# Optimization experiments

Hardware: AMD Instinct MI355X
Metric: run time of the kernel (lower is better)

## Reference

```python
import jax, jax.numpy as jnp
import numpy as np

E = 256   # embed_dim
L = 64    # num_landmarks
C = 256   # in_channels
N_ITER = 6


def iterative_inv(K):
    # Newton-Schulz pseudo-inverse on small [*, L, L] matrices (faithful to torch code)
    I = jnp.eye(K.shape[-1], dtype=K.dtype)
    KA = jnp.abs(K)
    V0 = KA.sum(axis=-2, keepdims=True).max(axis=-1, keepdims=True)  # [*,1,1]
    VI = KA.sum(axis=-1, keepdims=True).max(axis=-2, keepdims=True)  # [*,1,1]
    V = jnp.swapaxes(K, -1, -2) / (V0 * VI)
    for _ in range(N_ITER):
        KV = K @ V
        V = 0.25 * V @ (13.0 * I - KV @ (15.0 * I - KV @ (7.0 * I - KV)))
    return V


def setup_inputs() -> dict:
    key = jax.random.key(0)
    k0, k1, k2 = jax.random.split(key, 3)
    x = jax.random.normal(k0, (8, C, 64, 64), dtype=jnp.float32)
    # Conv2d 1x1 weights stored as [out, in]
    w_qkv = jax.random.normal(k1, (3 * E, C), dtype=jnp.float32) * 0.02
    b_qkv = jnp.zeros((3 * E,), dtype=jnp.float32)
    w_out = jax.random.normal(k2, (C, E), dtype=jnp.float32) * 0.02
    b_out = jnp.zeros((C,), dtype=jnp.float32)
    return {"x": x, "w_qkv": w_qkv, "b_qkv": b_qkv, "w_out": w_out, "b_out": b_out}


def reference(x, w_qkv, b_qkv, w_out, b_out):
    N, Cin, H, W = x.shape
    HW = H * W
    # 1x1 conv: [N, 3E, H, W]
    y = jnp.einsum('nchw,ec->nehw', x, w_qkv) + b_qkv[None, :, None, None]
    # faithful raw reshape (mixes channel/spatial like the torch code)
    qkv = y.reshape(N, HW, 3 * E)
    q, k, v = jnp.split(qkv, 3, axis=-1)                     # each [N, HW, E]
    scale = HW ** 0.5
    q_land = q.reshape(N, L, HW // L, E).mean(axis=-2) / scale  # [N, L, E]
    k_land = k.reshape(N, L, HW // L, E).mean(axis=-2) / scale  # [N, L, E]
    # three softmaxes, all over dim=-2 as in the original
    k1 = jax.nn.softmax(jnp.einsum('nie,nje->nij', q, k_land), axis=-2)       # [N, HW, L]
    k2 = jax.nn.softmax(jnp.einsum('nie,nje->nij', q_land, k_land), axis=-2)  # [N, L, L]
    k3 = jax.nn.softmax(jnp.einsum('nie,nje->nij', q_land, k), axis=-2)       # [N, L, HW]
    k2_inv = iterative_inv(k2)
    out = k1 @ (k2_inv @ (k3 @ v)) + v                        # [N, HW, E]
    out = out.reshape(N, E, H, W)                             # faithful raw reshape
    return jnp.einsum('nehw,ce->nchw', out, w_out) + b_out[None, :, None, None]
```

## Files before the change

### kernel.cpp

```cpp
#include <hip/hip_runtime.h>
#include <hip/hip_bf16.h>

typedef unsigned short u16;
typedef __attribute__((ext_vector_type(4))) float f32x4;
typedef __attribute__((ext_vector_type(8))) short short8;

#define NB   8
#define CIN  256
#define EDIM 256
#define M3   768
#define HWN  4096
#define LND  64
#define NS2  72

__device__ __forceinline__ float bf2f(u16 u){ return __uint_as_float(((unsigned)u)<<16); }
__device__ __forceinline__ u16 f2bf(float f){ __hip_bfloat16 h = __float2bfloat16(f); return *reinterpret_cast<u16*>(&h); }
__device__ __forceinline__ void bf2x2(unsigned u, float &lo, float &hi){
  lo = __uint_as_float(u<<16);
  hi = __uint_as_float(u & 0xffff0000u);
}

typedef __attribute__((address_space(1))) unsigned as1_uint;
typedef __attribute__((address_space(3))) unsigned as3_uint;
__device__ __forceinline__ void gl16(const void* g, void* l){
  __builtin_amdgcn_global_load_lds((const as1_uint*)g, (as3_uint*)l, 16, 0, 0);
}

__global__ __launch_bounds__(256) void k_prep(const float* __restrict__ x, u16* __restrict__ Xt,
                                              const float* __restrict__ wq, const float* __restrict__ wo,
                                              u16* __restrict__ Wqb, u16* __restrict__ Wob){
  const int bi = blockIdx.x;
  const int tid = threadIdx.x;
  if(bi >= 2048){
    int ti = (bi-2048)*256 + tid;
    const float* src; u16* dst;
    if(ti < 1536){ src = wq + (size_t)ti*128;        dst = Wqb + (size_t)ti*128; }
    else         { src = wo + (size_t)(ti-1536)*128; dst = Wob + (size_t)(ti-1536)*128; }
    #pragma unroll
    for(int t=0;t<128;t+=8){
      float4 v0 = *(const float4*)(src+t);
      float4 v1 = *(const float4*)(src+t+4);
      ushort4 o0, o1;
      o0.x=f2bf(v0.x); o0.y=f2bf(v0.y); o0.z=f2bf(v0.z); o0.w=f2bf(v0.w);
      o1.x=f2bf(v1.x); o1.y=f2bf(v1.y); o1.z=f2bf(v1.z); o1.w=f2bf(v1.w);
      *(ushort4*)(dst+t)   = o0;
      *(ushort4*)(dst+t+4) = o1;
    }
    return;
  }
  __shared__ float Ts[64*65];
  const int n = bi>>8, rem = bi&255, ct = rem>>6, pt = rem&63;
  const int c0 = ct*64, p0 = pt*64;
  {
    int cc = tid>>2, pj = (tid&3)*16;
    const float* xp = x + (size_t)n*CIN*HWN + (size_t)(c0+cc)*HWN + p0 + pj;
    #pragma unroll
    for(int j=0;j<16;j++) Ts[cc*65 + pj + j] = xp[j];
  }
  __syncthreads();
  {
    int pp = tid>>2, ej = (tid&3)*16;
    u16* op = Xt + ((size_t)n*HWN + p0 + pp)*CIN + c0 + ej;
    ushort4 o[4];
    #pragma unroll
    for(int j=0;j<16;j++) ((u16*)o)[j] = f2bf(Ts[(ej+j)*65 + pp]);
    *(ushort4*)(op+0)  = o[0];
    *(ushort4*)(op+4)  = o[1];
    *(ushort4*)(op+8)  = o[2];
    *(ushort4*)(op+12) = o[3];
  }
}

__global__ __launch_bounds__(256) void k_qkv(const u16* __restrict__ Wb, const u16* __restrict__ Xt,
                                             const float* __restrict__ bias, u16* __restrict__ Y){
  __shared__ __align__(16) u16 As[128*64];
  __shared__ __align__(16) u16 Bs[128*64];
  const int bi = blockIdx.x;
  const int n = bi&7, rem = bi>>3;
  const int ch0 = (rem%6)*128, p0 = (rem/6)*128;
  const int tid = threadIdx.x, lane = tid&63;
  const int c = tid&15, qq = (tid>>4)&3, w4 = tid>>6;
  const int wr0 = (w4&1)*64, wc0 = (w4>>1)*64;
  const u16* xb = Xt + ((size_t)n*HWN + p0)*CIN;
  const u16* wb = Wb + (size_t)ch0*CIN;
  f32x4 acc[4][4];
  #pragma unroll
  for(int mt=0;mt<4;mt++)
    #pragma unroll
    for(int nt=0;nt<4;nt++){ acc[mt][nt][0]=0.f; acc[mt][nt][1]=0.f; acc[mt][nt][2]=0.f; acc[mt][nt][3]=0.f; }
  const int srow  = w4*8 + (lane>>3);
  const int dslot = lane&7;
  const int sgo   = (dslot ^ (lane>>3))*8;
  const int rdswz = (c&7);
  for(int ph=0; ph<4; ph++){
    #pragma unroll
    for(int j=0;j<4;j++){
      int r = j*32 + srow;
      gl16(wb + (size_t)r*CIN + ph*64 + sgo, &As[r*64 + dslot*8]);
    }
    #pragma unroll
    for(int j=0;j<4;j++){
      int r = j*32 + srow;
      gl16(xb + (size_t)r*CIN + ph*64 + sgo, &Bs[r*64 + dslot*8]);
    }
    __syncthreads();
    #pragma unroll
    for(int kt=0;kt<2;kt++){
      short8 af[4], bff[4];
      const int rslot = ((kt*4+qq)^rdswz)*8;
      #pragma unroll
      for(int mt=0;mt<4;mt++) af[mt]  = *(const short8*)&As[(wr0+mt*16+c)*64 + rslot];
      #pragma unroll
      for(int nt=0;nt<4;nt++) bff[nt] = *(const short8*)&Bs[(wc0+nt*16+c)*64 + rslot];
      #pragma unroll
      for(int mt=0;mt<4;mt++)
        #pragma unroll
        for(int nt=0;nt<4;nt++)
          acc[mt][nt] = __builtin_amdgcn_mfma_f32_16x16x32_bf16(af[mt], bff[nt], acc[mt][nt], 0, 0, 0);
    }
    __syncthreads();
  }
  u16* Yb = Y + (size_t)n*M3*HWN;
  #pragma unroll
  for(int mt=0;mt<4;mt++){
    int chb = ch0 + wr0 + mt*16 + 4*qq;
    float b0 = bias[chb], b1 = bias[chb+1], b2 = bias[chb+2], b3 = bias[chb+3];
    #pragma unroll
    for(int nt=0;nt<4;nt++){
      int p = p0 + wc0 + nt*16 + c;
      u16* yp = Yb + (size_t)chb*HWN + p;
      yp[0]             = f2bf(acc[mt][nt][0]+b0);
      yp[HWN]           = f2bf(acc[mt][nt][1]+b1);
      yp[2*(size_t)HWN] = f2bf(acc[mt][nt][2]+b2);
      yp[3*(size_t)HWN] = f2bf(acc[mt][nt][3]+b3);
    }
  }
}

__global__ void k_land(const u16* __restrict__ Y, float* __restrict__ qland, float* __restrict__ kland){
  const int l = blockIdx.x, n = blockIdx.y, e = threadIdx.x;
  const u16* base = Y + (size_t)n*M3*HWN;
  float qs=0.f, ks=0.f;
  #pragma unroll 8
  for(int m=0;m<64;m++){
    size_t off = (size_t)(l*64+m)*M3;
    qs += bf2f(base[off+e]);
    ks += bf2f(base[off+256+e]);
  }
  qland[((size_t)n*LND+l)*EDIM+e] = qs*(1.f/4096.f);
  kland[((size_t)n*LND+l)*EDIM+e] = ks*(1.f/4096.f);
}

__device__ __forceinline__ void ns_mm2(const u16* L, int sL, const u16* Rt, int sR,
                                       int wv, int q, int c, f32x4 r4[4]){
  short8 a0 = *(const short8*)(L + (size_t)(16*wv + c)*sL + 8*q);
  short8 a1 = *(const short8*)(L + (size_t)(16*wv + c)*sL + 32 + 8*q);
  #pragma unroll
  for(int tc=0;tc<4;tc++){
    f32x4 acc = {0.f,0.f,0.f,0.f};
    short8 b0 = *(const short8*)(Rt + (size_t)(16*tc + c)*sR + 8*q);
    short8 b1 = *(const short8*)(Rt + (size_t)(16*tc + c)*sR + 32 + 8*q);
    acc = __builtin_amdgcn_mfma_f32_16x16x32_bf16(a0, b0, acc, 0, 0, 0);
    acc = __builtin_amdgcn_mfma_f32_16x16x32_bf16(a1, b1, acc, 0, 0, 0);
    r4[tc] = acc;
  }
}

#define TTS 64
__device__ void ns_body(int n, char* smem, const float* __restrict__ qland,
                        const float* __restrict__ kland, float* __restrict__ KinvT){
  u16* Kb  = (u16*)(smem + 0);
  u16* Vb  = (u16*)(smem + 9216);
  u16* Vt  = (u16*)(smem + 18432);
  u16* KVb = (u16*)(smem + 27648);
  u16* KVt = (u16*)(smem + 36864);
  u16* Tt  = (u16*)(smem + 46080);
  float* sS   = (float*)(smem + 27648);
  float* sred = (float*)(smem + 44544);
  const int tid = threadIdx.x;
  const int wv = tid>>6, q = (tid>>4)&3, c = tid&15;
  const float* qb = qland + (size_t)n*LND*EDIM;
  const float* kb = kland + (size_t)n*LND*EDIM;
  f32x4 acc[4];
  #pragma unroll
  for(int t=0;t<4;t++){ acc[t][0]=0.f; acc[t][1]=0.f; acc[t][2]=0.f; acc[t][3]=0.f; }
  for(int e0=0;e0<EDIM;e0+=64){
    __syncthreads();
    {
      int row = tid>>2, c0 = (tid&3)*16;
      const float* qp = qb + (size_t)row*EDIM + e0 + c0;
      const float* kp = kb + (size_t)row*EDIM + e0 + c0;
      u16* qd = &KVb[row*NS2 + c0];
      u16* kd = &KVt[row*NS2 + c0];
      #pragma unroll
      for(int j=0;j<16;j+=4){
        float4 qv = *(const float4*)(qp+j);
        float4 kv = *(const float4*)(kp+j);
        ushort4 qo, ko;
        qo.x=f2bf(qv.x); qo.y=f2bf(qv.y); qo.z=f2bf(qv.z); qo.w=f2bf(qv.w);
        ko.x=f2bf(kv.x); ko.y=f2bf(kv.y); ko.z=f2bf(kv.z); ko.w=f2bf(kv.w);
        *(ushort4*)(qd+j) = qo;
        *(ushort4*)(kd+j) = ko;
      }
    }
    __syncthreads();
    {
      short8 a0 = *(const short8*)&KVb[(16*wv+c)*NS2 + 8*q];
      short8 a1 = *(const short8*)&KVb[(16*wv+c)*NS2 + 32 + 8*q];
      #pragma unroll
      for(int tc=0;tc<4;tc++){
        short8 b0 = *(const short8*)&KVt[(16*tc+c)*NS2 + 8*q];
        short8 b1 = *(const short8*)&KVt[(16*tc+c)*NS2 + 32 + 8*q];
        acc[tc] = __builtin_amdgcn_mfma_f32_16x16x32_bf16(a0, b0, acc[tc], 0, 0, 0);
        acc[tc] = __builtin_amdgcn_mfma_f32_16x16x32_bf16(a1, b1, acc[tc], 0, 0, 0);
      }
    }
  }
  __syncthreads();
  #pragma unroll
  for(int tc=0;tc<4;tc++){
    int col = 16*tc + c, row0 = 16*wv + 4*q;
    sS[(row0+0)*66+col] = acc[tc][0];
    sS[(row0+1)*66+col] = acc[tc][1];
    sS[(row0+2)*66+col] = acc[tc][2];
    sS[(row0+3)*66+col] = acc[tc][3];
  }
  __syncthreads();
  if(tid < 64){
    int j = tid;
    float m = -1e30f;
    for(int i=0;i<64;i++) m = fmaxf(m, sS[i*66+j]);
    float ssum = 0.f;
    for(int i=0;i<64;i++) ssum += __expf(sS[i*66+j]-m);
    float inv = 1.f/ssum, cs = 0.f;
    for(int i=0;i<64;i++){
      float kv = __expf(sS[i*66+j]-m)*inv;
      cs += fabsf(kv);
      Kb[i*NS2+j] = f2bf(kv);
    }
    sred[j] = cs;
  }
  __syncthreads();
  if(tid < 64){
    int i = tid; float rs = 0.f;
    for(int j=0;j<64;j++) rs += fabsf(bf2f(Kb[i*NS2+j]));
    sred[64+i] = rs;
  }
  __syncthreads();
  if(tid == 0){
    float v0=-1e30f, vi=-1e30f;
    for(int t=0;t<64;t++){ v0 = fmaxf(v0, sred[t]); vi = fmaxf(vi, sred[64+t]); }
    sred[128] = 1.f/(v0*vi);
  }
  __syncthreads();
  {
    float sc = sred[128];
    int i = tid>>2, j16 = (tid&3)*16;
    #pragma unroll
    for(int jj=0;jj<16;jj++){
      int j = j16+jj;
      u16 bvv = f2bf(bf2f(Kb[j*NS2+i])*sc);
      Vb[i*NS2+j] = bvv;
      Vt[j*NS2+i] = bvv;
    }
  }
  __syncthreads();
  f32x4 r4[4];
  for(int it=0; it<6; it++){
    ns_mm2(Kb, NS2, Vt, NS2, wv, q, c, r4);
    #pragma unroll
    for(int tc=0;tc<4;tc++){
      int col = 16*tc + c, row0 = 16*wv + 4*q;
      ushort4 pk;
      pk.x = f2bf(r4[tc][0]); pk.y = f2bf(r4[tc][1]); pk.z = f2bf(r4[tc][2]); pk.w = f2bf(r4[tc][3]);
      KVb[(row0+0)*NS2+col] = pk.x; KVb[(row0+1)*NS2+col] = pk.y;
      KVb[(row0+2)*NS2+col] = pk.z; KVb[(row0+3)*NS2+col] = pk.w;
      *(ushort4*)&KVt[(size_t)col*NS2 + row0] = pk;
    }
    __syncthreads();
    ns_mm2(KVb, NS2, KVt, NS2, wv, q, c, r4);
    #pragma unroll
    for(int tc=0;tc<4;tc++){
      int col = 16*tc+c, row0 = 16*wv+4*q;
      ushort4 pk;
      #pragma unroll
      for(int r=0;r<4;r++){
        float kvv = bf2f(KVb[(row0+r)*NS2+col]);
        ((u16*)&pk)[r] = f2bf(7.f*kvv - r4[tc][r]);
      }
      *(ushort4*)&Tt[(size_t)col*TTS + row0] = pk;
    }
    __syncthreads();
    ns_mm2(KVb, NS2, Tt, TTS, wv, q, c, r4);
    __syncthreads();
    #pragma unroll
    for(int tc=0;tc<4;tc++){
      int col = 16*tc+c, row0 = 16*wv+4*q;
      ushort4 pk;
      #pragma unroll
      for(int r=0;r<4;r++){
        float kvv = bf2f(KVb[(row0+r)*NS2+col]);
        ((u16*)&pk)[r] = f2bf(15.f*kvv - r4[tc][r]);
      }
      *(ushort4*)&Tt[(size_t)col*TTS + row0] = pk;
    }
    __syncthreads();
    ns_mm2(Vb, NS2, Tt, TTS, wv, q, c, r4);
    __syncthreads();
    #pragma unroll
    for(int tc=0;tc<4;tc++){
      int col = 16*tc+c, row0 = 16*wv+4*q;
      float nv[4]; ushort4 pk;
      #pragma unroll
      for(int r=0;r<4;r++){
        float vv = bf2f(Vb[(row0+r)*NS2+col]);
        nv[r] = 0.25f*(13.f*vv - r4[tc][r]);
        u16 bb = f2bf(nv[r]);
        Vb[(row0+r)*NS2+col] = bb;
        ((u16*)&pk)[r] = bb;
      }
      *(ushort4*)&Vt[(size_t)col*NS2 + row0] = pk;
      if(it==5){
        *(float4*)&KinvT[(size_t)n*4096 + (size_t)col*64 + row0] = make_float4(nv[0],nv[1],nv[2],nv[3]);
      }
    }
    __syncthreads();
  }
}

#define LGS 264
__global__ __launch_bounds__(256) void k_landgemm(const u16* __restrict__ Y, const float* __restrict__ qland,
                                                  const float* __restrict__ kland, float* __restrict__ Z1,
                                                  float* __restrict__ Z3){
  __shared__ __align__(16) u16 As[64*LGS];
  __shared__ __align__(16) u16 BsU[2*64*64];
  const int z = blockIdx.y;
  const int n = z>>1, which = z&1;
  const int b0 = blockIdx.x*64;
  const float* land = (which ? qland : kland) + (size_t)n*LND*EDIM;
  const int boff = which ? 256 : 0;
  float* out = (which ? Z3 : Z1) + (size_t)n*LND*HWN;
  const u16* Yb = Y + (size_t)n*M3*HWN + boff;
  const int tid = threadIdx.x, lane = tid&63;
  const int c = tid&15, qq = (tid>>4)&3, wv = tid>>6;
  {
    int r = tid>>2, c0 = (tid&3)*64;
    const float* lp = land + (size_t)r*EDIM + c0;
    u16* dp = &As[r*LGS + c0];
    #pragma unroll
    for(int j=0;j<64;j+=4){
      float4 v = *(const float4*)(lp+j);
      ushort4 o; o.x=f2bf(v.x); o.y=f2bf(v.y); o.z=f2bf(v.z); o.w=f2bf(v.w);
      *(ushort4*)(dp+j) = o;
    }
  }
  const int srow  = wv*8 + (lane>>3);
  const int dslot = lane&7;
  const int sgo   = (dslot ^ (lane>>3))*8;
  const int rdswz = (c&7);
  f32x4 acc[4];
  #pragma unroll
  for(int nt=0;nt<4;nt++){ acc[nt][0]=0.f; acc[nt][1]=0.f; acc[nt][2]=0.f; acc[nt][3]=0.f; }
  #pragma unroll
  for(int j=0;j<2;j++){
    int r = j*32 + srow;
    gl16(Yb + (size_t)(b0+r)*M3 + sgo, BsU + r*64 + dslot*8);
  }
  __syncthreads();
  for(int ph=0; ph<4; ph++){
    const int cur = ph&1;
    if(ph<3){
      #pragma unroll
      for(int j=0;j<2;j++){
        int r = j*32 + srow;
        gl16(Yb + (size_t)(b0+r)*M3 + (ph+1)*64 + sgo, BsU + (cur^1)*4096 + r*64 + dslot*8);
      }
    }
    #pragma unroll
    for(int kt=0;kt<2;kt++){
      short8 af = *(const short8*)&As[(16*wv + c)*LGS + ph*64 + kt*32 + qq*8];
      const int rslot = ((kt*4+qq)^rdswz)*8;
      #pragma unroll
      for(int nt=0;nt<4;nt++){
        short8 bff = *(const short8*)&BsU[cur*4096 + (nt*16+c)*64 + rslot];
        acc[nt] = __builtin_amdgcn_mfma_f32_16x16x32_bf16(af, bff, acc[nt], 0, 0, 0);
      }
    }
    __syncthreads();
  }
  const int m0 = 16*wv + 4*qq;
  #pragma unroll
  for(int nt=0;nt<4;nt++){
    int col = b0 + nt*16 + c;
    out[(size_t)(m0+0)*HWN + col] = acc[nt][0];
    out[(size_t)(m0+1)*HWN + col] = acc[nt][1];
    out[(size_t)(m0+2)*HWN + col] = acc[nt][2];
    out[(size_t)(m0+3)*HWN + col] = acc[nt][3];
  }
}

__device__ void soft1_body(int b, char* smem, float* __restrict__ Z1){
  const int n = b>>6, j = b&63, tid = threadIdx.x;
  float* redm = (float*)smem;
  float* reds = redm + 4;
  float* base = Z1 + ((size_t)n*LND + j)*HWN;
  float v[16];
  float m = -1e30f;
  #pragma unroll
  for(int r=0;r<16;r++){ v[r] = base[r*256 + tid]; m = fmaxf(m, v[r]); }
  #pragma unroll
  for(int o=32;o;o>>=1) m = fmaxf(m, __shfl_xor(m, o));
  const int wid = tid>>6;
  if((tid&63)==0) redm[wid] = m;
  __syncthreads();
  m = fmaxf(fmaxf(redm[0],redm[1]), fmaxf(redm[2],redm[3]));
  float s = 0.f;
  #pragma unroll
  for(int r=0;r<16;r++){ v[r] = __expf(v[r]-m); s += v[r]; }
  #pragma unroll
  for(int o=32;o;o>>=1) s += __shfl_xor(s, o);
  if((tid&63)==0) reds[wid] = s;
  __syncthreads();
  s = reds[0]+reds[1]+reds[2]+reds[3];
  float inv = 1.f/s;
  #pragma unroll
  for(int r=0;r<16;r++) base[r*256 + tid] = v[r]*inv;
}

__global__ __launch_bounds__(256) void k_pv(const float* __restrict__ Z3, const u16* __restrict__ Y,
                                            float* __restrict__ part, float* __restrict__ Z1,
                                            const float* __restrict__ qland, const float* __restrict__ kland,
                                            float* __restrict__ KinvT){
  __shared__ __align__(16) char smem[54272];
  const int bi = blockIdx.x;
  if(bi < 8){ ns_body(bi, smem, qland, kland, KinvT); return; }
  if(bi >= 520){ soft1_body(bi-520, smem, Z1); return; }
  float* Sf   = (float*)smem;
  float* sinv = (float*)(smem + 33792);
  u16*   Asb  = (u16*)(smem + 34304);
  u16*   Vt   = (u16*)smem;
  const int idx = bi - 8;
  const int kc = idx&31, n = (idx>>5)&7, eh = idx>>8;
  const int jb = kc*128, eb = eh*128;
  const int tid = threadIdx.x, lane = tid&63;
  const int c = tid&15, qq = (tid>>4)&3, wv = tid>>6;
  const u16* Yb = Y + (size_t)n*M3*HWN;
  const float* z3b = Z3 + (size_t)n*LND*HWN;
  {
    int ibase = (tid>>5)*8, j4 = (tid&31)*4;
    #pragma unroll
    for(int r=0;r<8;r++){
      int i = ibase + r;
      *(float4*)&Sf[i*132 + j4] = *(const float4*)&z3b[(size_t)i*HWN + jb + j4];
    }
  }
  __syncthreads();
  if(tid < 128){
    int j = tid;
    float m = -1e30f;
    for(int i=0;i<64;i++) m = fmaxf(m, Sf[i*132 + j]);
    float s = 0.f;
    for(int i=0;i<64;i++){ float e = __expf(Sf[i*132 + j] - m); Sf[i*132 + j] = e; s += e; }
    sinv[j] = 1.f/s;
  }
  __syncthreads();
  {
    int i = tid>>2, j0q = (tid&3)*32;
    const int iswz = (i&7);
    #pragma unroll
    for(int t=0;t<32;t+=4){
      int jg = j0q + t;
      int phb = jg>>6, jl = jg&63;
      ushort4 o;
      o.x = f2bf(Sf[i*132 + jg+0]*sinv[jg+0]);
      o.y = f2bf(Sf[i*132 + jg+1]*sinv[jg+1]);
      o.z = f2bf(Sf[i*132 + jg+2]*sinv[jg+2]);
      o.w = f2bf(Sf[i*132 + jg+3]*sinv[jg+3]);
      *(ushort4*)&Asb[phb*4096 + i*64 + ((jl>>3)^iswz)*8 + (jl&7)] = o;
    }
  }
  __syncthreads();
  const int rdswz = (c&7);
  f32x4 acc[4][2];
  #pragma unroll
  for(int mt=0;mt<4;mt++)
    #pragma unroll
    for(int nt=0;nt<2;nt++){ acc[mt][nt][0]=0.f; acc[mt][nt][1]=0.f; acc[mt][nt][2]=0.f; acc[mt][nt][3]=0.f; }
  for(int ph=0; ph<2; ph++){
    #pragma unroll
    for(int rep=0; rep<4; rep++){
      int jl = (tid>>4) + 16*rep;
      int ec = (tid&15)*8;
      uint4 U = *(const uint4*)&Yb[(size_t)(jb+ph*64+jl)*M3 + 512 + eb + ec];
      const u16* uv = (const u16*)&U;
      #pragma unroll
      for(int k=0;k<8;k++){
        int e = ec+k;
        int slot = ((jl>>3) ^ (e&7) ^ ((e>>3)&7)) & 7;
        Vt[e*64 + slot*8 + (jl&7)] = uv[k];
      }
    }
    __syncthreads();
    #pragma unroll
    for(int kt=0;kt<2;kt++){
      const int rslotA = ((kt*4+qq)^rdswz)*8;
      short8 af[4];
      #pragma unroll
      for(int mt=0;mt<4;mt++) af[mt] = *(const short8*)&Asb[ph*4096 + (mt*16+c)*64 + rslotA];
      #pragma unroll
      for(int nt=0;nt<2;nt++){
        int e = wv*32 + nt*16 + c;
        int slotB = ((kt*4+qq) ^ (e&7) ^ ((e>>3)&7)) & 7;
        short8 bf_ = *(const short8*)&Vt[e*64 + slotB*8];
        #pragma unroll
        for(int mt=0;mt<4;mt++)
          acc[mt][nt] = __builtin_amdgcn_mfma_f32_16x16x32_bf16(af[mt], bf_, acc[mt][nt], 0, 0, 0);
      }
    }
    __syncthreads();
  }
  float* pb = part + ((size_t)n*32 + kc)*LND*EDIM + eb;
  #pragma unroll
  for(int mt=0;mt<4;mt++){
    int row0 = mt*16 + 4*qq;
    #pragma unroll
    for(int nt=0;nt<2;nt++){
      int e = wv*32 + nt*16 + c;
      pb[(size_t)(row0+0)*EDIM + e] = acc[mt][nt][0];
      pb[(size_t)(row0+1)*EDIM + e] = acc[mt][nt][1];
      pb[(size_t)(row0+2)*EDIM + e] = acc[mt][nt][2];
      pb[(size_t)(row0+3)*EDIM + e] = acc[mt][nt][3];
    }
  }
}

__global__ __launch_bounds__(256) void k_c2(const float* __restrict__ KinvT, const float* __restrict__ part,
                                            u16* __restrict__ C2T){
  const int eb = blockIdx.x*64, n = blockIdx.y, tid = threadIdx.x;
  __shared__ float KT[64][68];
  __shared__ float Bs2[64][68];
  __shared__ u16 Ct[64*72];
  {
    int l = tid>>2, o16 = (tid&3)*16;
    const float* kp = KinvT + (size_t)n*4096 + l*64 + o16;
    #pragma unroll
    for(int t=0;t<16;t+=4) *(float4*)&KT[l][o16+t] = *(const float4*)(kp+t);
    const float* pp = part + (size_t)n*32*16384 + (size_t)l*256 + eb + o16;
    float4 s0 = {0,0,0,0}, s1 = {0,0,0,0}, s2 = {0,0,0,0}, s3 = {0,0,0,0};
    for(int kc=0;kc<32;kc++){
      const float* b = pp + (size_t)kc*16384;
      float4 v0 = *(const float4*)(b);
      float4 v1 = *(const float4*)(b+4);
      float4 v2 = *(const float4*)(b+8);
      float4 v3 = *(const float4*)(b+12);
      s0.x+=v0.x; s0.y+=v0.y; s0.z+=v0.z; s0.w+=v0.w;
      s1.x+=v1.x; s1.y+=v1.y; s1.z+=v1.z; s1.w+=v1.w;
      s2.x+=v2.x; s2.y+=v2.y; s2.z+=v2.z; s2.w+=v2.w;
      s3.x+=v3.x; s3.y+=v3.y; s3.z+=v3.z; s3.w+=v3.w;
    }
    *(float4*)&Bs2[l][o16+0]  = s0;
    *(float4*)&Bs2[l][o16+4]  = s1;
    *(float4*)&Bs2[l][o16+8]  = s2;
    *(float4*)&Bs2[l][o16+12] = s3;
  }
  __syncthreads();
  const int j0 = (tid>>4)*4, u0 = (tid&15)*4;
  float acc[4][4] = {};
  #pragma unroll 8
  for(int l=0;l<64;l++){
    f32x4 a = *(f32x4*)&KT[l][j0];
    f32x4 b = *(f32x4*)&Bs2[l][u0];
    #pragma unroll
    for(int s=0;s<4;s++)
      #pragma unroll
      for(int u=0;u<4;u++) acc[s][u] += a[s]*b[u];
  }
  #pragma unroll
  for(int s=0;s<4;s++)
    #pragma unroll
    for(int u=0;u<4;u++)
      Ct[(u0+u)*72 + j0+s] = f2bf(acc[s][u]);
  __syncthreads();
  {
    int e = tid>>2, j16 = (tid&3)*16;
    u16* op = C2T + ((size_t)n*256 + eb + e)*64 + j16;
    #pragma unroll
    for(int t=0;t<16;t+=4)
      *(ushort4*)(op+t) = *(const ushort4*)&Ct[e*72 + j16 + t];
  }
}

__global__ __launch_bounds__(256) void k_out(const float* __restrict__ Z1, const u16* __restrict__ C2T,
                                             const u16* __restrict__ Y, u16* __restrict__ OM){
  __shared__ __align__(16) u16 Cs[256*64];
  __shared__ __align__(16) u16 Zt[64*72];
  const int ib = blockIdx.x*64, n = blockIdx.y;
  const int tid = threadIdx.x, lane = tid&63;
  const int c = tid&15, qq = (tid>>4)&3, wv = tid>>6;
  const int srow  = wv*8 + (lane>>3);
  const int dslot = lane&7;
  const int sgo   = (dslot ^ (lane>>3))*8;
  const int rdswz = (c&7);
  const u16* cb = C2T + (size_t)n*256*64;
  #pragma unroll
  for(int j=0;j<8;j++){
    int r = j*32 + srow;
    gl16(cb + (size_t)r*64 + sgo, &Cs[r*64 + dslot*8]);
  }
  {
    int j = tid>>2, i16 = (tid&3)*16;
    const float* zp = Z1 + ((size_t)n*LND + j)*HWN + ib + i16;
    #pragma unroll
    for(int t=0;t<16;t+=4){
      float4 v = *(const float4*)(zp+t);
      Zt[(i16+t+0)*72 + j] = f2bf(v.x);
      Zt[(i16+t+1)*72 + j] = f2bf(v.y);
      Zt[(i16+t+2)*72 + j] = f2bf(v.z);
      Zt[(i16+t+3)*72 + j] = f2bf(v.w);
    }
  }
  __syncthreads();
  f32x4 acc[4][4];
  #pragma unroll
  for(int mt=0;mt<4;mt++)
    #pragma unroll
    for(int nt=0;nt<4;nt++){ acc[mt][nt][0]=0.f; acc[mt][nt][1]=0.f; acc[mt][nt][2]=0.f; acc[mt][nt][3]=0.f; }
  #pragma unroll
  for(int kt=0;kt<2;kt++){
    const int rslot = ((kt*4+qq)^rdswz)*8;
    short8 af[4], bf_[4];
    #pragma unroll
    for(int mt=0;mt<4;mt++) af[mt] = *(const short8*)&Cs[(wv*64+mt*16+c)*64 + rslot];
    #pragma unroll
    for(int nt=0;nt<4;nt++) bf_[nt] = *(const short8*)&Zt[(nt*16+c)*72 + kt*32 + qq*8];
    #pragma unroll
    for(int mt=0;mt<4;mt++)
      #pragma unroll
      for(int nt=0;nt<4;nt++)
        acc[mt][nt] = __builtin_amdgcn_mfma_f32_16x16x32_bf16(af[mt], bf_[nt], acc[mt][nt], 0, 0, 0);
  }
  const u16* Yb = Y + (size_t)n*M3*HWN;
  u16* ob = OM + (size_t)n*HWN*EDIM;
  #pragma unroll
  for(int mt=0;mt<4;mt++){
    int e = wv*64 + mt*16 + 4*qq;
    #pragma unroll
    for(int nt=0;nt<4;nt++){
      int i = ib + nt*16 + c;
      ushort4 V4 = *(const ushort4*)(Yb + (size_t)i*M3 + 512 + e);
      ushort4 o;
      o.x = f2bf(acc[mt][nt][0] + bf2f(V4.x));
      o.y = f2bf(acc[mt][nt][1] + bf2f(V4.y));
      o.z = f2bf(acc[mt][nt][2] + bf2f(V4.z));
      o.w = f2bf(acc[mt][nt][3] + bf2f(V4.w));
      *(ushort4*)(ob + (size_t)i*EDIM + e) = o;
    }
  }
}

__global__ __launch_bounds__(256) void k_proj(const u16* __restrict__ Wb, const u16* __restrict__ OM,
                                              const float* __restrict__ bias, float* __restrict__ out){
  __shared__ __align__(16) u16 As[128*64];
  __shared__ __align__(16) u16 Bt[128*64];
  const int bi = blockIdx.x;
  const int n = bi&7, rem = bi>>3;
  const int ch0 = (rem&1)*128, p0 = (rem>>1)*128;
  const int tid = threadIdx.x, lane = tid&63;
  const int c = tid&15, qq = (tid>>4)&3, w4 = tid>>6;
  const int wr0 = (w4&1)*64, wc0 = (w4>>1)*64;
  const u16* omb = OM + (size_t)n*HWN*EDIM;
  const u16* wb = Wb + (size_t)ch0*EDIM;
  f32x4 acc[4][4];
  #pragma unroll
  for(int mt=0;mt<4;mt++)
    #pragma unroll
    for(int nt=0;nt<4;nt++){ acc[mt][nt][0]=0.f; acc[mt][nt][1]=0.f; acc[mt][nt][2]=0.f; acc[mt][nt][3]=0.f; }
  const int srow  = w4*8 + (lane>>3);
  const int dslot = lane&7;
  const int sgo   = (dslot ^ (lane>>3))*8;
  const int rdswz = (c&7);
  for(int ph=0; ph<4; ph++){
    #pragma unroll
    for(int j=0;j<4;j++){
      int r = j*32 + srow;
      gl16(wb + (size_t)r*EDIM + ph*64 + sgo, &As[r*64 + dslot*8]);
    }
    #pragma unroll
    for(int rep=0; rep<4; rep++){
      int ee = (tid>>4) + 16*rep;
      int pc = (tid&15)*8;
      uint4 U = *(const uint4*)&omb[(size_t)(ph*64+ee)*HWN + p0 + pc];
      const u16* uv = (const u16*)&U;
      #pragma unroll
      for(int k=0;k<8;k++){
        int p = pc+k;
        int slot = ((ee>>3) ^ (p&7) ^ ((p>>3)&7)) & 7;
        Bt[p*64 + slot*8 + (ee&7)] = uv[k];
      }
    }
    __syncthreads();
    #pragma unroll
    for(int kt=0;kt<2;kt++){
      const int rslot = ((kt*4+qq)^rdswz)*8;
      short8 af[4], bff[4];
      #pragma unroll
      for(int mt=0;mt<4;mt++) af[mt] = *(const short8*)&As[(wr0+mt*16+c)*64 + rslot];
      #pragma unroll
      for(int nt=0;nt<4;nt++){
        int p = wc0 + nt*16 + c;
        int slotB = ((kt*4+qq) ^ (p&7) ^ ((p>>3)&7)) & 7;
        bff[nt] = *(const short8*)&Bt[p*64 + slotB*8];
      }
      #pragma unroll
      for(int mt=0;mt<4;mt++)
        #pragma unroll
        for(int nt=0;nt<4;nt++)
          acc[mt][nt] = __builtin_amdgcn_mfma_f32_16x16x32_bf16(af[mt], bff[nt], acc[mt][nt], 0, 0, 0);
    }
    __syncthreads();
  }
  float* ob = out + (size_t)n*EDIM*HWN;
  #pragma unroll
  for(int mt=0;mt<4;mt++){
    int chb = ch0 + wr0 + mt*16 + 4*qq;
    float b0 = bias[chb], b1 = bias[chb+1], b2 = bias[chb+2], b3 = bias[chb+3];
    #pragma unroll
    for(int nt=0;nt<4;nt++){
      int p = p0 + wc0 + nt*16 + c;
      float* yp = ob + (size_t)chb*HWN + p;
      yp[0]             = acc[mt][nt][0]+b0;
      yp[HWN]           = acc[mt][nt][1]+b1;
      yp[2*(size_t)HWN] = acc[mt][nt][2]+b2;
      yp[3*(size_t)HWN] = acc[mt][nt][3]+b3;
    }
  }
}

extern "C" void kernel_launch(void* const* d_in, const int* in_sizes, int n_in,
                              void* d_out, int out_size, void* d_ws, size_t ws_size,
                              hipStream_t stream){
  (void)out_size; (void)ws_size;
  const float* x     = (const float*)d_in[0];
  const float* w_qkv = (const float*)d_in[1];
  const float* b_qkv = (const float*)d_in[2];
  const float* w_out = (const float*)d_in[3];
  const float* b_out = (const float*)d_in[4];
  for(int i=0;i<n_in;i++){
    switch(in_sizes[i]){
      case 8388608: x     = (const float*)d_in[i]; break;
      case 196608:  w_qkv = (const float*)d_in[i]; break;
      case 768:     b_qkv = (const float*)d_in[i]; break;
      case 65536:   w_out = (const float*)d_in[i]; break;
      case 256:     b_out = (const float*)d_in[i]; break;
      default: break;
    }
  }
  float* out = (float*)d_out;
  char* ws = (char*)d_ws;

  u16*   Y     = (u16*)(ws + 0);
  float* qland = (float*)(ws + 50331648);
  float* kland = (float*)(ws + 50855936);
  float* Z1    = (float*)(ws + 51380224);
  float* Z3    = (float*)(ws + 59768832);
  float* KinvT = (float*)(ws + 68157440);
  float* part  = (float*)(ws + 68288512);
  u16*   Xt    = (u16*)(ws + 68288512);
  u16*   C2T   = (u16*)(ws + 85065728);
  u16*   OM    = (u16*)(ws + 86114304);
  u16*   Wqb   = (u16*)(ws + 59768832);
  u16*   Wob   = (u16*)(ws + 102891520);

  k_prep    <<<dim3(2056),   256, 0, stream>>>(x, Xt, w_qkv, w_out, Wqb, Wob);
  k_qkv     <<<dim3(1536),   256, 0, stream>>>(Wqb, Xt, b_qkv, Y);
  k_land    <<<dim3(64,8),   256, 0, stream>>>(Y, qland, kland);
  k_landgemm<<<dim3(64,16),  256, 0, stream>>>(Y, qland, kland, Z1, Z3);
  k_pv      <<<dim3(1032),   256, 0, stream>>>(Z3, Y, part, Z1, qland, kland, KinvT);
  k_c2      <<<dim3(4,8),    256, 0, stream>>>(KinvT, part, C2T);
  k_out     <<<dim3(64,8),   256, 0, stream>>>(Z1, C2T, Y, OM);
  k_proj    <<<dim3(512),    256, 0, stream>>>(Wob, OM, b_out, out);
}
```

Before: 204.6 us.

## Split Newton-Schulz inverse across landgemm and pv kernels to shorten critical path

The serial 6-iteration Newton-Schulz inverse ran in 8 blocks inside k_pv, where it could be the long tail. It is now split in two: the first 3 iterations (including K2 softmax setup) run in extra blocks of k_landgemm, and the state (K and V in bf16) is saved to workspace. The remaining 3 iterations run in k_pv. The iteration body also drops two redundant __syncthreads and reuses the KVt buffer for the second temporary. This adds a workspace round trip and grows shared memory in k_landgemm to the union buffer size.

Measured after the change: 195.3 us. -4.5%, faster.

```diff
diff --git a/kernel.cpp b/kernel.cpp
--- a/kernel.cpp
+++ b/kernel.cpp
@@ -167,8 +167,70 @@
 }
 
 #define TTS 64
-__device__ void ns_body(int n, char* smem, const float* __restrict__ qland,
-                        const float* __restrict__ kland, float* __restrict__ KinvT){
+__device__ __forceinline__ void ns_iter(u16* Kb, u16* Vb, u16* Vt, u16* KVb, u16* KVt, u16* Tt,
+                                        int wv, int q, int c, bool last, int n,
+                                        float* __restrict__ KinvT){
+  f32x4 r4[4];
+  ns_mm2(Kb, NS2, Vt, NS2, wv, q, c, r4);
+  #pragma unroll
+  for(int tc=0;tc<4;tc++){
+    int col = 16*tc + c, row0 = 16*wv + 4*q;
+    ushort4 pk;
+    pk.x = f2bf(r4[tc][0]); pk.y = f2bf(r4[tc][1]); pk.z = f2bf(r4[tc][2]); pk.w = f2bf(r4[tc][3]);
+    KVb[(row0+0)*NS2+col] = pk.x; KVb[(row0+1)*NS2+col] = pk.y;
+    KVb[(row0+2)*NS2+col] = pk.z; KVb[(row0+3)*NS2+col] = pk.w;
+    *(ushort4*)&KVt[(size_t)col*NS2 + row0] = pk;
+  }
+  __syncthreads();
+  ns_mm2(KVb, NS2, KVt, NS2, wv, q, c, r4);
+  #pragma unroll
+  for(int tc=0;tc<4;tc++){
+    int col = 16*tc+c, row0 = 16*wv+4*q;
+    ushort4 pk;
+    #pragma unroll
+    for(int r=0;r<4;r++){
+      float kvv = bf2f(KVb[(row0+r)*NS2+col]);
+      ((u16*)&pk)[r] = f2bf(7.f*kvv - r4[tc][r]);
+    }
+    *(ushort4*)&Tt[(size_t)col*TTS + row0] = pk;
+  }
+  __syncthreads();
+  ns_mm2(KVb, NS2, Tt, TTS, wv, q, c, r4);
+  #pragma unroll
+  for(int tc=0;tc<4;tc++){
+    int col = 16*tc+c, row0 = 16*wv+4*q;
+    ushort4 pk;
+    #pragma unroll
+    for(int r=0;r<4;r++){
+      float kvv = bf2f(KVb[(row0+r)*NS2+col]);
+      ((u16*)&pk)[r] = f2bf(15.f*kvv - r4[tc][r]);
+    }
+    *(ushort4*)&KVt[(size_t)col*NS2 + row0] = pk;
+  }
+  __syncthreads();
+  ns_mm2(Vb, NS2, KVt, NS2, wv, q, c, r4);
+  #pragma unroll
+  for(int tc=0;tc<4;tc++){
+    int col = 16*tc+c, row0 = 16*wv+4*q;
+    float nv[4]; ushort4 pk;
+    #pragma unroll
+    for(int r=0;r<4;r++){
+      float vv = bf2f(Vb[(row0+r)*NS2+col]);
+      nv[r] = 0.25f*(13.f*vv - r4[tc][r]);
+      u16 bb = f2bf(nv[r]);
+      Vb[(row0+r)*NS2+col] = bb;
+      ((u16*)&pk)[r] = bb;
+    }
+    *(ushort4*)&Vt[(size_t)col*NS2 + row0] = pk;
+    if(last){
+      *(float4*)&KinvT[(size_t)n*4096 + (size_t)col*64 + row0] = make_float4(nv[0],nv[1],nv[2],nv[3]);
+    }
+  }
+  __syncthreads();
+}
+
+__device__ void ns_body_A(int n, char* smem, const float* __restrict__ qland,
+                          const float* __restrict__ kland, u16* __restrict__ NSst){
   u16* Kb  = (u16*)(smem + 0);
   u16* Vb  = (u16*)(smem + 9216);
   u16* Vt  = (u16*)(smem + 18432);
@@ -265,76 +327,62 @@
     }
   }
   __syncthreads();
-  f32x4 r4[4];
-  for(int it=0; it<6; it++){
-    ns_mm2(Kb, NS2, Vt, NS2, wv, q, c, r4);
-    #pragma unroll
-    for(int tc=0;tc<4;tc++){
-      int col = 16*tc + c, row0 = 16*wv + 4*q;
-      ushort4 pk;
-      pk.x = f2bf(r4[tc][0]); pk.y = f2bf(r4[tc][1]); pk.z = f2bf(r4[tc][2]); pk.w = f2bf(r4[tc][3]);
-      KVb[(row0+0)*NS2+col] = pk.x; KVb[(row0+1)*NS2+col] = pk.y;
-      KVb[(row0+2)*NS2+col] = pk.z; KVb[(row0+3)*NS2+col] = pk.w;
-      *(ushort4*)&KVt[(size_t)col*NS2 + row0] = pk;
-    }
-    __syncthreads();
-    ns_mm2(KVb, NS2, KVt, NS2, wv, q, c, r4);
-    #pragma unroll
-    for(int tc=0;tc<4;tc++){
-      int col = 16*tc+c, row0 = 16*wv+4*q;
-      ushort4 pk;
-      #pragma unroll
-      for(int r=0;r<4;r++){
-        float kvv = bf2f(KVb[(row0+r)*NS2+col]);
-        ((u16*)&pk)[r] = f2bf(7.f*kvv - r4[tc][r]);
-      }
-      *(ushort4*)&Tt[(size_t)col*TTS + row0] = pk;
-    }
-    __syncthreads();
-    ns_mm2(KVb, NS2, Tt, TTS, wv, q, c, r4);
-    __syncthreads();
-    #pragma unroll
-    for(int tc=0;tc<4;tc++){
-      int col = 16*tc+c, row0 = 16*wv+4*q;
-      ushort4 pk;
-      #pragma unroll
-      for(int r=0;r<4;r++){
-        float kvv = bf2f(KVb[(row0+r)*NS2+col]);
-        ((u16*)&pk)[r] = f2bf(15.f*kvv - r4[tc][r]);
-      }
-      *(ushort4*)&Tt[(size_t)col*TTS + row0] = pk;
-    }
-    __syncthreads();
-    ns_mm2(Vb, NS2, Tt, TTS, wv, q, c, r4);
-    __syncthreads();
-    #pragma unroll
-    for(int tc=0;tc<4;tc++){
-      int col = 16*tc+c, row0 = 16*wv+4*q;
-      float nv[4]; ushort4 pk;
-      #pragma unroll
-      for(int r=0;r<4;r++){
-        float vv = bf2f(Vb[(row0+r)*NS2+col]);
-        nv[r] = 0.25f*(13.f*vv - r4[tc][r]);
-        u16 bb = f2bf(nv[r]);
-        Vb[(row0+r)*NS2+col] = bb;
-        ((u16*)&pk)[r] = bb;
-      }
-      *(ushort4*)&Vt[(size_t)col*NS2 + row0] = pk;
-      if(it==5){
-        *(float4*)&KinvT[(size_t)n*4096 + (size_t)col*64 + row0] = make_float4(nv[0],nv[1],nv[2],nv[3]);
-      }
-    }
-    __syncthreads();
-  }
+  for(int it=0; it<3; it++)
+    ns_iter(Kb, Vb, Vt, KVb, KVt, Tt, wv, q, c, false, n, (float*)0);
+  {
+    int i = tid>>2, j16 = (tid&3)*16;
+    u16* kd = NSst + (size_t)n*4096 + i*64 + j16;
+    u16* vd = NSst + (size_t)(8+n)*4096 + i*64 + j16;
+    #pragma unroll
+    for(int t=0;t<16;t+=4){
+      *(ushort4*)(kd+t) = *(const ushort4*)&Kb[i*NS2 + j16 + t];
+      *(ushort4*)(vd+t) = *(const ushort4*)&Vb[i*NS2 + j16 + t];
+    }
+  }
+}
+
+__device__ void ns_body_B(int n, char* smem, const u16* __restrict__ NSst, float* __restrict__ KinvT){
+  u16* Kb  = (u16*)(smem + 0);
+  u16* Vb  = (u16*)(smem + 9216);
+  u16* Vt  = (u16*)(smem + 18432);
+  u16* KVb = (u16*)(smem + 27648);
+  u16* KVt = (u16*)(smem + 36864);
+  u16* Tt  = (u16*)(smem + 46080);
+  const int tid = threadIdx.x;
+  const int wv = tid>>6, q = (tid>>4)&3, c = tid&15;
+  {
+    int i = tid>>2, j16 = (tid&3)*16;
+    const u16* ks = NSst + (size_t)n*4096 + i*64 + j16;
+    const u16* vs = NSst + (size_t)(8+n)*4096 + i*64 + j16;
+    #pragma unroll
+    for(int t=0;t<16;t+=4){
+      ushort4 kk = *(const ushort4*)(ks+t);
+      ushort4 vv = *(const ushort4*)(vs+t);
+      *(ushort4*)&Kb[i*NS2 + j16 + t] = kk;
+      *(ushort4*)&Vb[i*NS2 + j16 + t] = vv;
+      Vt[(j16+t+0)*NS2 + i] = vv.x;
+      Vt[(j16+t+1)*NS2 + i] = vv.y;
+      Vt[(j16+t+2)*NS2 + i] = vv.z;
+      Vt[(j16+t+3)*NS2 + i] = vv.w;
+    }
+  }
+  __syncthreads();
+  for(int it=3; it<6; it++)
+    ns_iter(Kb, Vb, Vt, KVb, KVt, Tt, wv, q, c, it==5, n, KinvT);
 }
 
 #define LGS 264
 __global__ __launch_bounds__(256) void k_landgemm(const u16* __restrict__ Y, const float* __restrict__ qland,
                                                   const float* __restrict__ kland, float* __restrict__ Z1,
-                                                  float* __restrict__ Z3){
-  __shared__ __align__(16) u16 As[64*LGS];
-  __shared__ __align__(16) u16 BsU[2*64*64];
+                                                  float* __restrict__ Z3, u16* __restrict__ NSst){
+  __shared__ __align__(16) char usm[54272];
   const int z = blockIdx.y;
+  if(blockIdx.x == 64){
+    if((z&1)==0) ns_body_A(z>>1, usm, qland, kland, NSst);
+    return;
+  }
+  u16* As = (u16*)usm;
+  u16* BsU = (u16*)(usm + 33792);
   const int n = z>>1, which = z&1;
   const int b0 = blockIdx.x*64;
   const float* land = (which ? qland : kland) + (size_t)n*LND*EDIM;
@@ -429,11 +477,10 @@
 
 __global__ __launch_bounds__(256) void k_pv(const float* __restrict__ Z3, const u16* __restrict__ Y,
                                             float* __restrict__ part, float* __restrict__ Z1,
-                                            const float* __restrict__ qland, const float* __restrict__ kland,
-                                            float* __restrict__ KinvT){
+                                            const u16* __restrict__ NSst, float* __restrict__ KinvT){
   __shared__ __align__(16) char smem[54272];
   const int bi = blockIdx.x;
-  if(bi < 8){ ns_body(bi, smem, qland, kland, KinvT); return; }
+  if(bi < 8){ ns_body_B(bi, smem, NSst, KinvT); return; }
   if(bi >= 520){ soft1_body(bi-520, smem, Z1); return; }
   float* Sf   = (float*)smem;
   float* sinv = (float*)(smem + 33792);
@@ -767,6 +814,7 @@
   float* part  = (float*)(ws + 68288512);
   u16*   Xt    = (u16*)(ws + 68288512);
   u16*   C2T   = (u16*)(ws + 85065728);
+  u16*   NSst  = (u16*)(ws + 85327872);
   u16*   OM    = (u16*)(ws + 86114304);
   u16*   Wqb   = (u16*)(ws + 59768832);
   u16*   Wob   = (u16*)(ws + 102891520);
@@ -774,8 +822,8 @@
   k_prep    <<<dim3(2056),   256, 0, stream>>>(x, Xt, w_qkv, w_out, Wqb, Wob);
   k_qkv     <<<dim3(1536),   256, 0, stream>>>(Wqb, Xt, b_qkv, Y);
   k_land    <<<dim3(64,8),   256, 0, stream>>>(Y, qland, kland);
-  k_landgemm<<<dim3(64,16),  256, 0, stream>>>(Y, qland, kland, Z1, Z3);
-  k_pv      <<<dim3(1032),   256, 0, stream>>>(Z3, Y, part, Z1, qland, kland, KinvT);
+  k_landgemm<<<dim3(65,16),  256, 0, stream>>>(Y, qland, kland, Z1, Z3, NSst);
+  k_pv      <<<dim3(1032),   256, 0, stream>>>(Z3, Y, part, Z1, NSst, KinvT);
   k_c2      <<<dim3(4,8),    256, 0, stream>>>(KinvT, part, C2T);
   k_out     <<<dim3(64,8),   256, 0, stream>>>(Z1, C2T, Y, OM);
   k_proj    <<<dim3(512),    256, 0, stream>>>(Wob, OM, b_out, out);
```
